# Performance work log

Hardware: AMD Instinct MI355X
Metric: run time of the kernel (lower is better)

## Reference

```python
import jax, jax.numpy as jnp
from jax import lax
import numpy as np


def setup_inputs() -> dict:
    key = jax.random.key(0)
    k1, k2 = jax.random.split(key)
    sat_features = jax.random.normal(k1, (128, 4, 64, 16), dtype=jnp.float32)  # [B_s, h, w, c]
    grd_features = jax.random.normal(k2, (128, 4, 64, 16), dtype=jnp.float32)  # [B_g, h, gw, c]
    return {"sat_features": sat_features, "grd_features": grd_features}


def reference(sat_features, grd_features):
    B_s, h, w, c = sat_features.shape
    B_g, gh, gw, gc = grd_features.shape
    assert h == gh and c == gc

    # --- corr: circular cross-correlation over width via conv2d ---
    n = gw - 1
    sat_pad = jnp.concatenate([sat_features, sat_features[:, :, :n, :]], axis=2)  # [B_s,h,w+n,c]
    rhs = jnp.transpose(grd_features, (1, 2, 3, 0))  # HWIO: [h,gw,c,B_g]
    out = lax.conv_general_dilated(
        sat_pad, rhs, window_strides=(1, 1), padding='VALID',
        dimension_numbers=('NHWC', 'HWIO', 'NHWC'))  # [B_s,1,w,B_g]
    corr = out[:, 0, :, :]                  # [B_s, w, B_g]
    orien = jnp.argmax(corr, axis=1)        # [B_s, B_g] int

    # --- crop_sat: circular-shift gather along width, crop to grd width ---
    shift = orien % w                                                   # [B_s,B_g]
    idx = (jnp.arange(gw)[None, None, :] + shift[:, :, None]) % w       # [B_s,B_g,gw]
    # gather: sat_crop[i,j,y,k,ch] = sat_features[i, y, idx[i,j,k], ch]
    sat_crop = jnp.take_along_axis(
        sat_features[:, None],              # [B_s,1,h,w,c]
        idx[:, :, None, :, None],           # [B_s,B_g,1,gw,1]
        axis=3)                             # -> [B_s,B_g,h,gw,c]

    # --- L2 normalize per (sat,grd) pair and squared-chord distance ---
    norm = jnp.sqrt(jnp.sum(sat_crop * sat_crop, axis=(2, 3, 4), keepdims=True))
    sat_matrix = sat_crop / jnp.maximum(norm, 1e-12)
    dot = jnp.sum(sat_matrix * grd_features[None], axis=(2, 3, 4))      # [B_s,B_g]
    distance = 2.0 - 2.0 * dot.T                                        # [B_g,B_s]

    return sat_features, grd_features, distance, orien
```

## Files before the change

kernel.cpp:

```cpp
#include <hip/hip_runtime.h>
#include <math.h>

typedef _Float16 f16;
typedef __attribute__((ext_vector_type(8))) _Float16 f16x8;
typedef __attribute__((ext_vector_type(16))) float f32x16;

#define DIST_OFF  1048576
#define ORI_OFF   1064960
#define SATP_STR  72
#define RSTR      66

#define MFMA(a,b,c) __builtin_amdgcn_mfma_f32_32x32x16_f16((a),(b),(c),0,0,0)

__global__ __launch_bounds__(256) void prep_k(const float* __restrict__ grd,
                                              f16* __restrict__ gHi, f16* __restrict__ gLo) {
    __shared__ f16 tH[8192], tL[8192];
    const int b = blockIdx.x;
    const int tid = threadIdx.x;
    const int g0 = (b & 7) * 16;
    const int kq = b >> 3;
    #pragma unroll
    for (int i = 0; i < 32; ++i) {
        int flat = i * 256 + tid;
        int g_l = flat >> 9;
        int r   = flat & 511;
        int h   = r >> 7;
        int j   = r & 127;
        float v = grd[(((g0 + g_l) * 4 + h) * 64 + kq * 8) * 16 + j];
        int k_l = (j >> 4) * 64 + h * 16 + (j & 15);
        f16 hv = (f16)v;
        int a = (k_l >> 3) * 128 + g_l * 8 + (k_l & 7);
        tH[a] = hv;
        tL[a] = (f16)(v - (float)hv);
    }
    __syncthreads();
    #pragma unroll
    for (int i = 0; i < 4; ++i) {
        int f = i * 256 + tid;
        int dst = (kq * 64 + (f >> 4)) * 128 + g0 + (f & 15);
        ((f16x8*)gHi)[dst] = *(const f16x8*)(tH + f * 8);
        ((f16x8*)gLo)[dst] = *(const f16x8*)(tL + f * 8);
    }
}

__global__ __launch_bounds__(1024, 4) void corr_k(const float* __restrict__ sat,
                                                  const f16* __restrict__ gHi,
                                                  const f16* __restrict__ gLo,
                                                  float* __restrict__ out,
                                                  const float4* __restrict__ satIn,
                                                  const float4* __restrict__ grdIn,
                                                  int fuse) {
    __shared__ __align__(16) unsigned char smem[135168];
    __shared__ float wred[16];
    __shared__ float rnormS;
    f16* sH = (f16*)smem;
    f16* sL = sH + 127 * SATP_STR;
    float* red = (float*)smem;

    const int tid = threadIdx.x;
    const int s  = blockIdx.x >> 1;
    const int gh = blockIdx.x & 1;
    const int wave = tid >> 6, lane = tid & 63;
    const int m = lane & 31, half = lane >> 5;

    if (fuse && tid < 512) {
        float4* o4 = (float4*)out;
        int i = blockIdx.x * 512 + tid;
        o4[i] = satIn[i];
        o4[131072 + i] = grdIn[i];
    }

    const float* satS = sat + s * 4096;
    float ssq = 0.f;
    #pragma unroll
    for (int r = 0; r < 4; ++r) {
        int idx = r * 1024 + tid;
        float v = satS[idx];
        int h = idx >> 10, w = (idx >> 4) & 63, c = idx & 15;
        int col = h * 16 + c;
        f16 hv = (f16)v, lv = (f16)(v - (float)hv);
        sH[w * SATP_STR + col] = hv;
        sL[w * SATP_STR + col] = lv;
        if (w < 63) { sH[(w + 64) * SATP_STR + col] = hv; sL[(w + 64) * SATP_STR + col] = lv; }
        ssq += v * v;
    }
    #pragma unroll
    for (int off = 32; off > 0; off >>= 1) ssq += __shfl_down(ssq, off, 64);
    if (lane == 0) wred[wave] = ssq;
    __syncthreads();
    if (tid == 0) {
        float t = 0.f;
        #pragma unroll
        for (int i = 0; i < 16; ++i) t += wred[i];
        rnormS = 1.f / fmaxf(sqrtf(t), 1e-12f);
    }

    const f16* Ah = sH + m * SATP_STR + half * 8;
    const f16* Al = sL + m * SATP_STR + half * 8;
    const f16x8* BH = (const f16x8*)gHi + half * 128 + gh * 64 + m;
    const f16x8* BL = (const f16x8*)gLo + half * 128 + gh * 64 + m;

    f32x16 acc[2][2];
    #pragma unroll
    for (int jt = 0; jt < 2; ++jt)
        #pragma unroll
        for (int gt = 0; gt < 2; ++gt)
            #pragma unroll
            for (int r = 0; r < 16; ++r) acc[jt][gt][r] = 0.f;

    const int t0 = wave * 16;
    const int rot = (wave & 3) * 4;
    #pragma unroll 4
    for (int i = 0; i < 16; ++i) {
        int t = t0 + ((i + rot) & 15);
        int ao = (t >> 2) * SATP_STR + (t & 3) * 16;
        f16x8 ah0 = *(const f16x8*)(Ah + ao);
        f16x8 ah1 = *(const f16x8*)(Ah + ao + 32 * SATP_STR);
        f16x8 al0 = *(const f16x8*)(Al + ao);
        f16x8 al1 = *(const f16x8*)(Al + ao + 32 * SATP_STR);
        int bu = t * 256;
        f16x8 bh0 = BH[bu], bh1 = BH[bu + 32];
        f16x8 bl0 = BL[bu], bl1 = BL[bu + 32];
        acc[0][0] = MFMA(ah0, bh0, acc[0][0]);
        acc[0][1] = MFMA(ah0, bh1, acc[0][1]);
        acc[1][0] = MFMA(ah1, bh0, acc[1][0]);
        acc[1][1] = MFMA(ah1, bh1, acc[1][1]);
        acc[0][0] = MFMA(ah0, bl0, acc[0][0]);
        acc[0][1] = MFMA(ah0, bl1, acc[0][1]);
        acc[1][0] = MFMA(ah1, bl0, acc[1][0]);
        acc[1][1] = MFMA(ah1, bl1, acc[1][1]);
        acc[0][0] = MFMA(al0, bh0, acc[0][0]);
        acc[0][1] = MFMA(al0, bh1, acc[0][1]);
        acc[1][0] = MFMA(al1, bh0, acc[1][0]);
        acc[1][1] = MFMA(al1, bh1, acc[1][1]);
    }

    __syncthreads();
#define PUT(rp, op) { \
    _Pragma("unroll") for (int jt = 0; jt < 2; ++jt) \
    _Pragma("unroll") for (int gt = 0; gt < 2; ++gt) { \
        float* row = (rp) + (gt * 32 + m) * RSTR + jt * 32 + half * 4; \
        _Pragma("unroll") for (int q = 0; q < 4; ++q) { \
            float2 u = { acc[jt][gt][4*q], acc[jt][gt][4*q+1] }; \
            float2 v = { acc[jt][gt][4*q+2], acc[jt][gt][4*q+3] }; \
            op(row + q * 8, u, v); } } }
#define OPW(p, u, v)  { *(float2*)(p) = u; *(float2*)((p) + 2) = v; }
#define OPA(p, u, v)  { float2 a = *(float2*)(p), b = *(float2*)((p) + 2); \
                        a.x += u.x; a.y += u.y; b.x += v.x; b.y += v.y; \
                        *(float2*)(p) = a; *(float2*)((p) + 2) = b; }

    if (wave >= 8) PUT(red + (wave - 8) * 4224, OPW)
    __syncthreads();
    if (wave < 8)  PUT(red + wave * 4224, OPA)
    __syncthreads();
    {
        int g = tid >> 4, q4 = (tid & 15) * 4;
        int base = g * RSTR + q4;
        float2 u = {0.f, 0.f}, v = {0.f, 0.f};
        #pragma unroll
        for (int kh = 0; kh < 8; ++kh) {
            float2 a = *(const float2*)(red + kh * 4224 + base);
            float2 b = *(const float2*)(red + kh * 4224 + base + 2);
            u.x += a.x; u.y += a.y; v.x += b.x; v.y += b.y;
        }
        *(float2*)(red + base) = u;
        *(float2*)(red + base + 2) = v;
    }
    __syncthreads();

    if (tid < 64) {
        int g = tid;
        const float* row = red + g * RSTR;
        float best = row[0];
        int bj = 0;
        for (int j = 1; j < 64; ++j) {
            float v = row[j];
            if (v > best) { best = v; bj = j; }
        }
        float dot = best * rnormS;
        int gg = gh * 64 + g;
        out[DIST_OFF + gg * 128 + s] = 2.f - 2.f * dot;
        out[ORI_OFF + s * 128 + gg]  = (float)bj;
    }
}

__global__ void copy_k(const float4* __restrict__ a, const float4* __restrict__ b,
                       float4* __restrict__ out) {
    int i = blockIdx.x * 256 + threadIdx.x;
    out[i] = a[i];
    out[131072 + i] = b[i];
}

extern "C" void kernel_launch(void* const* d_in, const int* in_sizes, int n_in,
                              void* d_out, int out_size, void* d_ws, size_t ws_size,
                              hipStream_t stream) {
    const float* sat = (const float*)d_in[0];
    const float* grd = (const float*)d_in[1];
    float* out = (float*)d_out;

    const bool useWs = (ws_size >= (size_t)2 * 1024 * 1024);
    f16* gHi;
    f16* gLo;
    if (useWs) {
        gHi = (f16*)d_ws;
        gLo = gHi + 524288;
    } else {
        gHi = (f16*)out;
        gLo = (f16*)(out + 262144);
    }

    prep_k<<<64, 256, 0, stream>>>(grd, gHi, gLo);
    corr_k<<<256, 1024, 0, stream>>>(sat, gHi, gLo, out,
                                     (const float4*)sat, (const float4*)grd,
                                     useWs ? 1 : 0);
    if (!useWs)
        copy_k<<<512, 256, 0, stream>>>((const float4*)sat, (const float4*)grd, (float4*)out);
}
```

Measured before the change: 88.11 us.

## Split waves across output tiles instead of K slices to shrink reduction

Each wave now owns one 32x32 output tile (jt, gt) and one quarter of the K range, instead of all four tiles over a sixteenth of K. This cuts the per-wave accumulators from four to two, halves the LDS reduction buffer, and drops one reduction pass and barrier. In exchange each wave issues fewer MFMAs per A/B load, so operand reuse falls and global B loads per MFMA rise. The accumulation chain per wave also gets longer.

```diff
diff --git a/kernel.cpp b/kernel.cpp
--- a/kernel.cpp
+++ b/kernel.cpp
@@ -50,7 +50,7 @@
                                                   const float4* __restrict__ satIn,
                                                   const float4* __restrict__ grdIn,
                                                   int fuse) {
-    __shared__ __align__(16) unsigned char smem[135168];
+    __shared__ __align__(16) unsigned char smem[67584];
     __shared__ float wred[16];
     __shared__ float rnormS;
     f16* sH = (f16*)smem;
@@ -62,6 +62,7 @@
     const int gh = blockIdx.x & 1;
     const int wave = tid >> 6, lane = tid & 63;
     const int m = lane & 31, half = lane >> 5;
+    const int jt = wave & 1, gt = (wave >> 1) & 1, kh = wave >> 2;
 
     if (fuse && tid < 512) {
         float4* o4 = (float4*)out;
@@ -95,72 +96,49 @@
         rnormS = 1.f / fmaxf(sqrtf(t), 1e-12f);
     }
 
-    const f16* Ah = sH + m * SATP_STR + half * 8;
-    const f16* Al = sL + m * SATP_STR + half * 8;
-    const f16x8* BH = (const f16x8*)gHi + half * 128 + gh * 64 + m;
-    const f16x8* BL = (const f16x8*)gLo + half * 128 + gh * 64 + m;
+    const f16* Ah = sH + (jt * 32 + m) * SATP_STR + half * 8;
+    const f16* Al = sL + (jt * 32 + m) * SATP_STR + half * 8;
+    const f16x8* BH = (const f16x8*)gHi + half * 128 + gh * 64 + gt * 32 + m;
+    const f16x8* BL = (const f16x8*)gLo + half * 128 + gh * 64 + gt * 32 + m;
 
-    f32x16 acc[2][2];
+    f32x16 accH, accX;
     #pragma unroll
-    for (int jt = 0; jt < 2; ++jt)
-        #pragma unroll
-        for (int gt = 0; gt < 2; ++gt)
-            #pragma unroll
-            for (int r = 0; r < 16; ++r) acc[jt][gt][r] = 0.f;
+    for (int r = 0; r < 16; ++r) { accH[r] = 0.f; accX[r] = 0.f; }
 
-    const int t0 = wave * 16;
-    const int rot = (wave & 3) * 4;
+    const int t0 = kh * 64;
     #pragma unroll 4
-    for (int i = 0; i < 16; ++i) {
-        int t = t0 + ((i + rot) & 15);
+    for (int t = t0; t < t0 + 64; ++t) {
         int ao = (t >> 2) * SATP_STR + (t & 3) * 16;
-        f16x8 ah0 = *(const f16x8*)(Ah + ao);
-        f16x8 ah1 = *(const f16x8*)(Ah + ao + 32 * SATP_STR);
-        f16x8 al0 = *(const f16x8*)(Al + ao);
-        f16x8 al1 = *(const f16x8*)(Al + ao + 32 * SATP_STR);
-        int bu = t * 256;
-        f16x8 bh0 = BH[bu], bh1 = BH[bu + 32];
-        f16x8 bl0 = BL[bu], bl1 = BL[bu + 32];
-        acc[0][0] = MFMA(ah0, bh0, acc[0][0]);
-        acc[0][1] = MFMA(ah0, bh1, acc[0][1]);
-        acc[1][0] = MFMA(ah1, bh0, acc[1][0]);
-        acc[1][1] = MFMA(ah1, bh1, acc[1][1]);
-        acc[0][0] = MFMA(ah0, bl0, acc[0][0]);
-        acc[0][1] = MFMA(ah0, bl1, acc[0][1]);
-        acc[1][0] = MFMA(ah1, bl0, acc[1][0]);
-        acc[1][1] = MFMA(ah1, bl1, acc[1][1]);
-        acc[0][0] = MFMA(al0, bh0, acc[0][0]);
-        acc[0][1] = MFMA(al0, bh1, acc[0][1]);
-        acc[1][0] = MFMA(al1, bh0, acc[1][0]);
-        acc[1][1] = MFMA(al1, bh1, acc[1][1]);
+        f16x8 ah = *(const f16x8*)(Ah + ao);
+        f16x8 al = *(const f16x8*)(Al + ao);
+        f16x8 bh = BH[t * 256];
+        f16x8 bl = BL[t * 256];
+        accH = MFMA(ah, bh, accH);
+        accX = MFMA(ah, bl, accX);
+        accX = MFMA(al, bh, accX);
     }
+    accH = accH + accX;
 
     __syncthreads();
-#define PUT(rp, op) { \
-    _Pragma("unroll") for (int jt = 0; jt < 2; ++jt) \
-    _Pragma("unroll") for (int gt = 0; gt < 2; ++gt) { \
-        float* row = (rp) + (gt * 32 + m) * RSTR + jt * 32 + half * 4; \
-        _Pragma("unroll") for (int q = 0; q < 4; ++q) { \
-            float2 u = { acc[jt][gt][4*q], acc[jt][gt][4*q+1] }; \
-            float2 v = { acc[jt][gt][4*q+2], acc[jt][gt][4*q+3] }; \
-            op(row + q * 8, u, v); } } }
-#define OPW(p, u, v)  { *(float2*)(p) = u; *(float2*)((p) + 2) = v; }
-#define OPA(p, u, v)  { float2 a = *(float2*)(p), b = *(float2*)((p) + 2); \
-                        a.x += u.x; a.y += u.y; b.x += v.x; b.y += v.y; \
-                        *(float2*)(p) = a; *(float2*)((p) + 2) = b; }
-
-    if (wave >= 8) PUT(red + (wave - 8) * 4224, OPW)
-    __syncthreads();
-    if (wave < 8)  PUT(red + wave * 4224, OPA)
+    {
+        float* row = red + kh * 4224 + (gt * 32 + m) * RSTR + jt * 32 + half * 4;
+        #pragma unroll
+        for (int q = 0; q < 4; ++q) {
+            float2 u = { accH[4 * q],     accH[4 * q + 1] };
+            float2 v = { accH[4 * q + 2], accH[4 * q + 3] };
+            *(float2*)(row + q * 8)     = u;
+            *(float2*)(row + q * 8 + 2) = v;
+        }
+    }
     __syncthreads();
     {
         int g = tid >> 4, q4 = (tid & 15) * 4;
         int base = g * RSTR + q4;
         float2 u = {0.f, 0.f}, v = {0.f, 0.f};
         #pragma unroll
-        for (int kh = 0; kh < 8; ++kh) {
-            float2 a = *(const float2*)(red + kh * 4224 + base);
-            float2 b = *(const float2*)(red + kh * 4224 + base + 2);
+        for (int k = 0; k < 4; ++k) {
+            float2 a = *(const float2*)(red + k * 4224 + base);
+            float2 b = *(const float2*)(red + k * 4224 + base + 2);
             u.x += a.x; u.y += a.y; v.x += b.x; v.y += b.y;
         }
         *(float2*)(red + base) = u;
```

Result: slower. 92.25 us (+4.7%).
